# Kernel tuning notes

Hardware: AMD Instinct MI355X
Metric: run time of the kernel (lower is better)

## Reference

```python
import jax, jax.numpy as jnp
import numpy as np

N = 100000
E = 1250000
H = 64


def setup_inputs() -> dict:
    key = jax.random.key(0)
    ks = jax.random.split(key, 20)
    x = jax.random.normal(ks[0], (N, 1), dtype=jnp.float32)
    edge_index = jax.random.randint(ks[1], (2, E), 0, N, dtype=jnp.int64)
    edge_attr = jax.random.uniform(ks[2], (E,), dtype=jnp.float32)
    def lin(k, fin, fout):
        s = 1.0 / np.sqrt(fin)
        kw, kb = jax.random.split(k)
        W = jax.random.uniform(kw, (fin, fout), minval=-s, maxval=s, dtype=jnp.float32)
        b = jax.random.uniform(kb, (fout,), minval=-s, maxval=s, dtype=jnp.float32)
        return W, b
    W1, b1 = lin(ks[3], 1, H)
    W2, b2 = lin(ks[4], H, H)
    W3, b3 = lin(ks[5], H, H)
    W4, b4 = lin(ks[6], H, H)
    W5, b5 = lin(ks[7], H, H)
    fW1, fb1 = lin(ks[8], H, H)
    fW2, fb2 = lin(ks[9], H, 1)
    return dict(x=x, edge_index=edge_index, edge_attr=edge_attr,
                W1=W1, b1=b1, W2=W2, b2=b2, W3=W3, b3=b3, W4=W4, b4=b4,
                W5=W5, b5=b5, fW1=fW1, fb1=fb1, fW2=fW2, fb2=fb2)


def _gcn_layer(x, W, b, src, dst, ew):
    # PyG GCNConv: x' = D^{-1/2}(A+I)D^{-1/2} x W + b (self-loops pre-appended)
    h = x @ W                                   # [N, H]
    deg = jax.ops.segment_sum(ew, dst, num_segments=N)
    dinv = jnp.where(deg > 0, jax.lax.rsqrt(deg), 0.0)
    norm = dinv[src] * ew * dinv[dst]           # [E+N]
    msg = h[src] * norm[:, None]                # [E+N, H]
    return jax.ops.segment_sum(msg, dst, num_segments=N) + b


def reference(x, edge_index, edge_attr, W1, b1, W2, b2, W3, b3, W4, b4, W5, b5, fW1, fb1, fW2, fb2):
    loops = jnp.arange(N, dtype=edge_index.dtype)
    src = jnp.concatenate([edge_index[0], loops])
    dst = jnp.concatenate([edge_index[1], loops])
    ew = jnp.concatenate([edge_attr, jnp.ones((N,), edge_attr.dtype)])
    h = jax.nn.relu(_gcn_layer(x, W1, b1, src, dst, ew))
    h = jax.nn.relu(_gcn_layer(h, W2, b2, src, dst, ew))
    h = jax.nn.relu(_gcn_layer(h, W3, b3, src, dst, ew))
    h = jax.nn.relu(_gcn_layer(h, W4, b4, src, dst, ew))
    h = jax.nn.relu(_gcn_layer(h, W5, b5, src, dst, ew))
    h = jax.nn.relu(h @ fW1 + fb1)
    return h @ fW2 + fb2
```

## Files before the change

kernel.cpp:

```cpp
#include <hip/hip_runtime.h>
#include <hip/hip_bf16.h>

#define NN 100000
#define EE 1250000

#define RL(x, l) __builtin_amdgcn_readlane((x), (l))
#define RLF(x, l) __int_as_float(__builtin_amdgcn_readlane(__float_as_int(x), (l)))

typedef __attribute__((ext_vector_type(8))) short v8s;
typedef __attribute__((ext_vector_type(4))) float v4f;
typedef __attribute__((ext_vector_type(4))) unsigned int v4u;

__device__ __forceinline__ unsigned short bf16rtn(float x) {
    unsigned u = __float_as_uint(x);
    unsigned r = u + 0x7fffu + ((u >> 16) & 1u);
    return (unsigned short)(r >> 16);
}
__device__ __forceinline__ unsigned bf16rtn2(float lo, float hi) {
    return (unsigned)bf16rtn(lo) | ((unsigned)bf16rtn(hi) << 16);
}
__device__ __forceinline__ float bflo(unsigned u) { return __uint_as_float(u << 16); }
__device__ __forceinline__ float bfhi(unsigned u) { return __uint_as_float(u & 0xffff0000u); }
__device__ __forceinline__ float bfs(unsigned short s) { return __uint_as_float((unsigned)s << 16); }


__global__ __launch_bounds__(256) void k_count(const int* __restrict__ ei,
                                               const float* __restrict__ ew,
                                               unsigned long long* __restrict__ cnt,
                                               int* __restrict__ slot) {
    int e = blockIdx.x * 256 + threadIdx.x;
    if (e >= EE) return;
    int d = __builtin_nontemporal_load(&ei[EE + e]);
    float w = __builtin_nontemporal_load(&ew[e]);
    unsigned fx = (unsigned)(w * 16777216.0f + 0.5f);
    unsigned long long old =
        atomicAdd(&cnt[d], (1ULL << 32) | (unsigned long long)fx);
    __builtin_nontemporal_store((int)(old >> 32), &slot[e]);
}

__global__ __launch_bounds__(256) void k_bsum(const unsigned long long* __restrict__ cnt,
                                              int* __restrict__ bsum) {
    __shared__ int ls[256];
    int b = blockIdx.x, tid = threadIdx.x;
    int base = b * 1024 + tid * 4;
    int s = 0;
    #pragma unroll
    for (int j = 0; j < 4; ++j) { int g = base + j; if (g < NN) s += (int)(cnt[g] >> 32); }
    ls[tid] = s; __syncthreads();
    for (int off = 128; off > 0; off >>= 1) {
        if (tid < off) ls[tid] += ls[tid + off];
        __syncthreads();
    }
    if (tid == 0) bsum[b] = ls[0];
}

__global__ __launch_bounds__(256) void k_scan_out(const unsigned long long* __restrict__ cnt,
                                                  const int* __restrict__ bsum,
                                                  const float* __restrict__ x,
                                                  int* __restrict__ rowptr,
                                                  float* __restrict__ dinv,
                                                  float* __restrict__ xd) {
    __shared__ int ls[256];
    __shared__ int sbase;
    int b = blockIdx.x, tid = threadIdx.x;
    if (tid < 64) {
        int w0 = (tid < b) ? bsum[tid] : 0;
        int w1 = ((64 + tid) < b) ? bsum[64 + tid] : 0;
        int s = w0 + w1;
        #pragma unroll
        for (int m = 32; m >= 1; m >>= 1) s += __shfl_xor(s, m, 64);
        if (tid == 0) sbase = s;
    }
    int base = b * 1024 + tid * 4;
    int c[4]; float sw[4]; int s = 0;
    #pragma unroll
    for (int j = 0; j < 4; ++j) {
        int g = base + j;
        unsigned long long v = (g < NN) ? cnt[g] : 0ULL;
        c[j] = (int)(v >> 32);
        sw[j] = (float)(unsigned)(v & 0xffffffffu) * (1.0f / 16777216.0f);
        s += c[j];
    }
    ls[tid] = s; __syncthreads();
    for (int off = 1; off < 256; off <<= 1) {
        int v = (tid >= off) ? ls[tid - off] : 0;
        __syncthreads();
        ls[tid] += v;
        __syncthreads();
    }
    int excl = ls[tid] - s + sbase;
    #pragma unroll
    for (int j = 0; j < 4; ++j) {
        int g = base + j;
        if (g < NN) {
            rowptr[g + 1] = excl + c[j];
            excl += c[j];
            float di = rsqrtf(sw[j] + 1.0f);
            dinv[g] = di;
            xd[g] = di * x[g];
        }
    }
    if (b == 0 && tid == 0) rowptr[0] = 0;
}

__global__ __launch_bounds__(256) void k_fill(const int* __restrict__ ei,
                                              const float* __restrict__ ew,
                                              const int* __restrict__ slot,
                                              const int* __restrict__ rowptr,
                                              int2* __restrict__ epair) {
    int e = blockIdx.x * 256 + threadIdx.x;
    if (e >= EE) return;
    int s = __builtin_nontemporal_load(&ei[e]);
    int d = __builtin_nontemporal_load(&ei[EE + e]);
    float w = __builtin_nontemporal_load(&ew[e]);
    int sl = __builtin_nontemporal_load(&slot[e]);
    int p = rowptr[d] + sl;
    epair[p] = make_int2(s, __float_as_int(w));
}

__global__ __launch_bounds__(256) void k_wpk(const float* __restrict__ Wa,
                                             const float* __restrict__ Wb,
                                             const float* __restrict__ Wc,
                                             const float* __restrict__ Wd,
                                             unsigned* __restrict__ Wf) {
    const float* W = (blockIdx.x == 0) ? Wa : (blockIdx.x == 1) ? Wb
                   : (blockIdx.x == 2) ? Wc : Wd;
    unsigned* out = Wf + blockIdx.x * 4096;
    int t = threadIdx.x;
    #pragma unroll
    for (int i = 0; i < 2; ++i) {
        int s = t * 2 + i;
        int lane = s & 63;
        int nt = (s >> 6) & 3;
        int kt = s >> 8;
        int col = nt * 16 + (lane & 15);
        int k0 = kt * 32 + (lane >> 4) * 8;
        unsigned hi[4], lo[4];
        #pragma unroll
        for (int d = 0; d < 4; ++d) {
            float w0 = W[(k0 + 2 * d) * 64 + col];
            float w1 = W[(k0 + 2 * d + 1) * 64 + col];
            unsigned short h0 = bf16rtn(w0), h1 = bf16rtn(w1);
            float r0 = w0 - bfs(h0), r1 = w1 - bfs(h1);
            hi[d] = (unsigned)h0 | ((unsigned)h1 << 16);
            lo[d] = (unsigned)bf16rtn(r0) | ((unsigned)bf16rtn(r1) << 16);
        }
        int gh = (0 * 2 + kt) * 4 + nt;
        int gl = (1 * 2 + kt) * 4 + nt;
        *(v4u*)&out[(gh * 64 + lane) * 4] = (v4u){hi[0], hi[1], hi[2], hi[3]};
        *(v4u*)&out[(gl * 64 + lane) * 4] = (v4u){lo[0], lo[1], lo[2], lo[3]};
    }
}


__global__ __launch_bounds__(256) void k_l1(
    const float* __restrict__ xd, const float* __restrict__ dinv,
    const int* __restrict__ rowptr, const int2* __restrict__ ep,
    const float* __restrict__ W1, const float* __restrict__ b1,
    const float* __restrict__ W2, unsigned short* __restrict__ Gout)
{
    __shared__ float sW[4096];
    int tid = threadIdx.x;
    #pragma unroll
    for (int i = 0; i < 16; ++i) sW[tid + i * 256] = W2[tid + i * 256];
    __syncthreads();
    int lane = tid & 63, l16 = lane & 15, sub = lane >> 4;
    int g4 = blockIdx.x * 4 + (tid >> 6);
    int nodeS = g4 * 4 + sub;
    int beg = rowptr[nodeS], end = rowptr[nodeS + 1];
    float partial = 0.f;
    for (int idx = beg + l16; idx < end; idx += 16) {
        int2 p = ep[idx];
        partial = fmaf(__int_as_float(p.y), xd[p.x], partial);
    }
    #pragma unroll
    for (int m = 8; m >= 1; m >>= 1) partial += __shfl_xor(partial, m, 64);
    float z = dinv[nodeS] * (xd[nodeS] + partial);
    float z0 = RLF(z, 0), z1 = RLF(z, 16), z2 = RLF(z, 32), z3 = RLF(z, 48);
    float w1l = W1[lane], b1l = b1[lane];
    float v0 = fmaxf(fmaf(z0, w1l, b1l), 0.f);
    float v1 = fmaxf(fmaf(z1, w1l, b1l), 0.f);
    float v2 = fmaxf(fmaf(z2, w1l, b1l), 0.f);
    float v3 = fmaxf(fmaf(z3, w1l, b1l), 0.f);
    float a0 = 0.f, a1 = 0.f, a2 = 0.f, a3 = 0.f;
    #pragma unroll
    for (int k = 0; k < 64; ++k) {
        float wk = sW[k * 64 + lane];
        a0 = fmaf(RLF(v0, k), wk, a0);
        a1 = fmaf(RLF(v1, k), wk, a1);
        a2 = fmaf(RLF(v2, k), wk, a2);
        a3 = fmaf(RLF(v3, k), wk, a3);
    }
    int n0 = g4 * 4;
    Gout[(n0 + 0) * 64 + lane] = bf16rtn(dinv[n0 + 0] * a0);
    Gout[(n0 + 1) * 64 + lane] = bf16rtn(dinv[n0 + 1] * a1);
    Gout[(n0 + 2) * 64 + lane] = bf16rtn(dinv[n0 + 2] * a2);
    Gout[(n0 + 3) * 64 + lane] = bf16rtn(dinv[n0 + 3] * a3);
}

__global__ __launch_bounds__(256) void k_gmv(
    const unsigned* __restrict__ G16, const float* __restrict__ dinv,
    const int* __restrict__ rowptr, const int2* __restrict__ ep,
    const float* __restrict__ bias, const unsigned* __restrict__ Wf,
    unsigned short* __restrict__ Gout)
{
    __shared__ __align__(16) unsigned sB[4096];
    __shared__ __align__(16) unsigned sA[4][128];
    int tid = threadIdx.x;
    #pragma unroll
    for (int i = 0; i < 4; ++i)
        ((v4u*)sB)[tid + i * 256] = ((const v4u*)Wf)[tid + i * 256];
    int lane = tid & 63;
    int wid  = tid >> 6;
    int lc   = lane & 31;
    int half = lane >> 5;
    int n0 = (blockIdx.x * 4 + wid) * 4;
    float2 bb = ((const float2*)bias)[lc];
    for (int r = 0; r < 4; ++r) {
        int node = n0 + r;
        int beg = __builtin_amdgcn_readfirstlane(rowptr[node]);
        int end = __builtin_amdgcn_readfirstlane(rowptr[node + 1]);
        float ax = 0.f, ay = 0.f;
        if (half == 0) {
            unsigned u = G16[node * 32 + lc];
            ax = bflo(u); ay = bfhi(u);
        }
        int j = beg;
        for (; j + 16 <= end; j += 16) {
            unsigned u[8]; float nv[8];
            #pragma unroll
            for (int t = 0; t < 8; ++t) {
                int2 pa = ep[j + t];
                int2 pb = ep[j + 8 + t];
                int src = half ? pb.x : pa.x;
                nv[t] = __int_as_float(half ? pb.y : pa.y);
                u[t] = G16[src * 32 + lc];
            }
            #pragma unroll
            for (int t = 0; t < 8; ++t) {
                ax = fmaf(bflo(u[t]), nv[t], ax);
                ay = fmaf(bfhi(u[t]), nv[t], ay);
            }
        }
        if (j < end) {
            unsigned u[8]; float nv[8];
            #pragma unroll
            for (int t = 0; t < 8; ++t) {
                int ia = j + t, ib = j + 8 + t;
                int2 pa = ep[ia < end ? ia : j];
                int2 pb = ep[ib < end ? ib : j];
                int src = half ? pb.x : pa.x;
                float w = __int_as_float(half ? pb.y : pa.y);
                bool v = half ? (ib < end) : (ia < end);
                nv[t] = v ? w : 0.f;
                u[t] = G16[src * 32 + lc];
            }
            #pragma unroll
            for (int t = 0; t < 8; ++t) {
                ax = fmaf(bflo(u[t]), nv[t], ax);
                ay = fmaf(bfhi(u[t]), nv[t], ay);
            }
        }
        ax += __shfl_xor(ax, 32, 64);
        ay += __shfl_xor(ay, 32, 64);
        float din = dinv[node];
        float ve = fmaxf(fmaf(din, ax, bb.x), 0.f);
        float vo = fmaxf(fmaf(din, ay, bb.y), 0.f);
        if (half == 0) sA[wid][r * 32 + lc] = bf16rtn2(ve, vo);
    }
    __syncthreads();
    int rr  = lane & 3;
    int blk = lane >> 4;
    v8s a0 = *(const v8s*)&sA[wid][rr * 32 +  0 + blk * 4];
    v8s a1 = *(const v8s*)&sA[wid][rr * 32 + 16 + blk * 4];
    v4f acc[4];
    #pragma unroll
    for (int nt = 0; nt < 4; ++nt) {
        v8s bh0 = *(const v8s*)&sB[((0 * 4 + nt) * 64 + lane) * 4];
        v8s bh1 = *(const v8s*)&sB[((1 * 4 + nt) * 64 + lane) * 4];
        v8s bl0 = *(const v8s*)&sB[((2 * 4 + nt) * 64 + lane) * 4];
        v8s bl1 = *(const v8s*)&sB[((3 * 4 + nt) * 64 + lane) * 4];
        v4f c = {0.f, 0.f, 0.f, 0.f};
        c = __builtin_amdgcn_mfma_f32_16x16x32_bf16(a0, bl0, c, 0, 0, 0);
        c = __builtin_amdgcn_mfma_f32_16x16x32_bf16(a1, bl1, c, 0, 0, 0);
        c = __builtin_amdgcn_mfma_f32_16x16x32_bf16(a0, bh0, c, 0, 0, 0);
        c = __builtin_amdgcn_mfma_f32_16x16x32_bf16(a1, bh1, c, 0, 0, 0);
        acc[nt] = c;
    }
    if (lane < 16) {
        float4 dn = *(const float4*)&dinv[n0];
        #pragma unroll
        for (int r = 0; r < 4; ++r) {
            float d = (r == 0) ? dn.x : (r == 1) ? dn.y : (r == 2) ? dn.z : dn.w;
            #pragma unroll
            for (int nt = 0; nt < 4; ++nt)
                Gout[(n0 + r) * 64 + nt * 16 + lane] = bf16rtn(d * acc[nt][r]);
        }
    }
}

__global__ __launch_bounds__(256) void k_ghead(
    const unsigned* __restrict__ G16, const float* __restrict__ dinv,
    const int* __restrict__ rowptr, const int2* __restrict__ ep,
    const float* __restrict__ b5, const unsigned* __restrict__ Wf,
    const float* __restrict__ fb1, const float* __restrict__ fW2,
    const float* __restrict__ fb2, float* __restrict__ out)
{
    __shared__ __align__(16) unsigned sB[4096];
    __shared__ __align__(16) unsigned sA[4][128];
    int tid = threadIdx.x;
    #pragma unroll
    for (int i = 0; i < 4; ++i)
        ((v4u*)sB)[tid + i * 256] = ((const v4u*)Wf)[tid + i * 256];
    int lane = tid & 63;
    int wid  = tid >> 6;
    int lc   = lane & 31;
    int half = lane >> 5;
    int n0 = (blockIdx.x * 4 + wid) * 4;
    float2 bb = ((const float2*)b5)[lc];
    int l16 = lane & 15;
    float fb1v[4], fw2v[4];
    #pragma unroll
    for (int nt = 0; nt < 4; ++nt) {
        fb1v[nt] = fb1[nt * 16 + l16];
        fw2v[nt] = fW2[nt * 16 + l16];
    }
    float fb2s = fb2[0];
    for (int r = 0; r < 4; ++r) {
        int node = n0 + r;
        int beg = __builtin_amdgcn_readfirstlane(rowptr[node]);
        int end = __builtin_amdgcn_readfirstlane(rowptr[node + 1]);
        float ax = 0.f, ay = 0.f;
        if (half == 0) {
            unsigned u = G16[node * 32 + lc];
            ax = bflo(u); ay = bfhi(u);
        }
        int j = beg;
        for (; j + 16 <= end; j += 16) {
            unsigned u[8]; float nv[8];
            #pragma unroll
            for (int t = 0; t < 8; ++t) {
                int2 pa = ep[j + t];
                int2 pb = ep[j + 8 + t];
                int src = half ? pb.x : pa.x;
                nv[t] = __int_as_float(half ? pb.y : pa.y);
                u[t] = G16[src * 32 + lc];
            }
            #pragma unroll
            for (int t = 0; t < 8; ++t) {
                ax = fmaf(bflo(u[t]), nv[t], ax);
                ay = fmaf(bfhi(u[t]), nv[t], ay);
            }
        }
        if (j < end) {
            unsigned u[8]; float nv[8];
            #pragma unroll
            for (int t = 0; t < 8; ++t) {
                int ia = j + t, ib = j + 8 + t;
                int2 pa = ep[ia < end ? ia : j];
                int2 pb = ep[ib < end ? ib : j];
                int src = half ? pb.x : pa.x;
                float w = __int_as_float(half ? pb.y : pa.y);
                bool v = half ? (ib < end) : (ia < end);
                nv[t] = v ? w : 0.f;
                u[t] = G16[src * 32 + lc];
            }
            #pragma unroll
            for (int t = 0; t < 8; ++t) {
                ax = fmaf(bflo(u[t]), nv[t], ax);
                ay = fmaf(bfhi(u[t]), nv[t], ay);
            }
        }
        ax += __shfl_xor(ax, 32, 64);
        ay += __shfl_xor(ay, 32, 64);
        float din = dinv[node];
        float ve = fmaxf(fmaf(din, ax, bb.x), 0.f);
        float vo = fmaxf(fmaf(din, ay, bb.y), 0.f);
        if (half == 0) sA[wid][r * 32 + lc] = bf16rtn2(ve, vo);
    }
    __syncthreads();
    int rr  = lane & 3;
    int blk = lane >> 4;
    v8s a0 = *(const v8s*)&sA[wid][rr * 32 +  0 + blk * 4];
    v8s a1 = *(const v8s*)&sA[wid][rr * 32 + 16 + blk * 4];
    v4f acc[4];
    #pragma unroll
    for (int nt = 0; nt < 4; ++nt) {
        v8s bh0 = *(const v8s*)&sB[((0 * 4 + nt) * 64 + lane) * 4];
        v8s bh1 = *(const v8s*)&sB[((1 * 4 + nt) * 64 + lane) * 4];
        v8s bl0 = *(const v8s*)&sB[((2 * 4 + nt) * 64 + lane) * 4];
        v8s bl1 = *(const v8s*)&sB[((3 * 4 + nt) * 64 + lane) * 4];
        v4f c = {0.f, 0.f, 0.f, 0.f};
        c = __builtin_amdgcn_mfma_f32_16x16x32_bf16(a0, bl0, c, 0, 0, 0);
        c = __builtin_amdgcn_mfma_f32_16x16x32_bf16(a1, bl1, c, 0, 0, 0);
        c = __builtin_amdgcn_mfma_f32_16x16x32_bf16(a0, bh0, c, 0, 0, 0);
        c = __builtin_amdgcn_mfma_f32_16x16x32_bf16(a1, bh1, c, 0, 0, 0);
        acc[nt] = c;
    }
    float tr[4];
    #pragma unroll
    for (int r = 0; r < 4; ++r) {
        float t = 0.f;
        #pragma unroll
        for (int nt = 0; nt < 4; ++nt)
            t += fmaxf(acc[nt][r] + fb1v[nt], 0.f) * fw2v[nt];
        #pragma unroll
        for (int m = 8; m >= 1; m >>= 1) t += __shfl_xor(t, m, 64);
        tr[r] = t;
    }
    if (lane == 0) {
        float4 o = {tr[0] + fb2s, tr[1] + fb2s, tr[2] + fb2s, tr[3] + fb2s};
        *(float4*)&out[n0] = o;
    }
}


extern "C" void kernel_launch(void* const* d_in, const int* in_sizes, int n_in,
                              void* d_out, int out_size, void* d_ws, size_t ws_size,
                              hipStream_t stream) {
    const float* x   = (const float*)d_in[0];
    const int*   ei  = (const int*)d_in[1];
    const float* ew  = (const float*)d_in[2];
    const float* W1  = (const float*)d_in[3];
    const float* b1  = (const float*)d_in[4];
    const float* W2  = (const float*)d_in[5];
    const float* b2  = (const float*)d_in[6];
    const float* W3  = (const float*)d_in[7];
    const float* b3  = (const float*)d_in[8];
    const float* W4  = (const float*)d_in[9];
    const float* b4  = (const float*)d_in[10];
    const float* W5  = (const float*)d_in[11];
    const float* b5  = (const float*)d_in[12];
    const float* fW1 = (const float*)d_in[13];
    const float* fb1 = (const float*)d_in[14];
    const float* fW2 = (const float*)d_in[15];
    const float* fb2 = (const float*)d_in[16];
    float* out = (float*)d_out;

    char* ws = (char*)d_ws;
    size_t o = 0;
    auto alloc = [&](size_t elems) -> void* {
        void* p = (void*)(ws + o);
        o += ((elems * 4 + 255) / 256) * 256;
        return p;
    };
    float* dinv   = (float*)alloc(NN);
    float* xd     = (float*)alloc(NN);
    int*   rowptr = (int*)alloc(NN + 1);
    unsigned long long* cnt64 = (unsigned long long*)alloc(2 * (size_t)NN);
    int*   bsum   = (int*)alloc(128);
    int2*  epair  = (int2*)alloc(2 * (size_t)EE);
    unsigned* Ga16 = (unsigned*)alloc((size_t)NN * 32);
    unsigned* Gb16 = (unsigned*)alloc((size_t)NN * 32);
    int*   slot   = (int*)alloc(EE);
    unsigned* Wf  = (unsigned*)alloc(4 * 4096);

    int gE  = (EE + 255) / 256;
    int nb  = (NN + 1023) / 1024;
    int gW4 = NN / 16;

    k_wpk<<<4, 256, 0, stream>>>(W3, W4, W5, fW1, Wf);
    hipMemsetAsync(cnt64, 0, NN * sizeof(unsigned long long), stream);
    k_count<<<gE, 256, 0, stream>>>(ei, ew, cnt64, slot);
    k_bsum<<<nb, 256, 0, stream>>>(cnt64, bsum);
    k_scan_out<<<nb, 256, 0, stream>>>(cnt64, bsum, x, rowptr, dinv, xd);
    k_fill<<<gE, 256, 0, stream>>>(ei, ew, slot, rowptr, epair);

    k_l1<<<gW4, 256, 0, stream>>>(xd, dinv, rowptr, epair, W1, b1, W2,
                                  (unsigned short*)Ga16);
    k_gmv<<<gW4, 256, 0, stream>>>(Ga16, dinv, rowptr, epair, b2, Wf + 0,
                                   (unsigned short*)Gb16);
    k_gmv<<<gW4, 256, 0, stream>>>(Gb16, dinv, rowptr, epair, b3, Wf + 4096,
                                   (unsigned short*)Ga16);
    k_gmv<<<gW4, 256, 0, stream>>>(Ga16, dinv, rowptr, epair, b4, Wf + 8192,
                                   (unsigned short*)Gb16);
    k_ghead<<<gW4, 256, 0, stream>>>(Gb16, dinv, rowptr, epair, b5, Wf + 12288,
                                     fb1, fW2, fb2, out);
}
```

Before: 428.0 us.

## Gather four nodes concurrently per wave with 16 lanes each and 8-byte loads

The aggregation in the middle layers and the head kernel is restructured. Each wave now processes its four nodes in parallel, one 16-lane quarter per node, with each lane loading 4 bf16 features (uint2). Before, the wave walked the nodes one after another, split edges across two 32-lane halves, and combined them with a cross-half shuffle. The aim is more memory parallelism and no serial per-node loop, at the cost of divergent loop trip counts when neighbouring nodes have different degrees.

```diff
diff --git a/kernel.cpp b/kernel.cpp
--- a/kernel.cpp
+++ b/kernel.cpp
@@ -152,6 +152,50 @@
     }
 }
 
+__device__ __forceinline__ void gatherq(
+    const unsigned* __restrict__ G16, const int2* __restrict__ ep,
+    int node, int beg, int end, int l16,
+    float& a0, float& a1, float& a2, float& a3)
+{
+    uint2 su = *(const uint2*)&G16[node * 32 + l16 * 2];
+    a0 = bflo(su.x); a1 = bfhi(su.x);
+    a2 = bflo(su.y); a3 = bfhi(su.y);
+    int j = beg;
+    for (; j + 8 <= end; j += 8) {
+        uint2 u[8]; float nv[8];
+        #pragma unroll
+        for (int t = 0; t < 8; ++t) {
+            int2 p = ep[j + t];
+            nv[t] = __int_as_float(p.y);
+            u[t] = *(const uint2*)&G16[p.x * 32 + l16 * 2];
+        }
+        #pragma unroll
+        for (int t = 0; t < 8; ++t) {
+            a0 = fmaf(bflo(u[t].x), nv[t], a0);
+            a1 = fmaf(bfhi(u[t].x), nv[t], a1);
+            a2 = fmaf(bflo(u[t].y), nv[t], a2);
+            a3 = fmaf(bfhi(u[t].y), nv[t], a3);
+        }
+    }
+    if (j < end) {
+        uint2 u[8]; float nv[8];
+        #pragma unroll
+        for (int t = 0; t < 8; ++t) {
+            int idx = j + t;
+            int2 p = ep[idx < end ? idx : j];
+            nv[t] = (idx < end) ? __int_as_float(p.y) : 0.f;
+            u[t] = *(const uint2*)&G16[p.x * 32 + l16 * 2];
+        }
+        #pragma unroll
+        for (int t = 0; t < 8; ++t) {
+            a0 = fmaf(bflo(u[t].x), nv[t], a0);
+            a1 = fmaf(bfhi(u[t].x), nv[t], a1);
+            a2 = fmaf(bflo(u[t].y), nv[t], a2);
+            a3 = fmaf(bfhi(u[t].y), nv[t], a3);
+        }
+    }
+}
+
 
 __global__ __launch_bounds__(256) void k_l1(
     const float* __restrict__ xd, const float* __restrict__ dinv,
@@ -212,67 +256,26 @@
         ((v4u*)sB)[tid + i * 256] = ((const v4u*)Wf)[tid + i * 256];
     int lane = tid & 63;
     int wid  = tid >> 6;
-    int lc   = lane & 31;
-    int half = lane >> 5;
+    int q    = lane >> 4;
+    int l16  = lane & 15;
     int n0 = (blockIdx.x * 4 + wid) * 4;
-    float2 bb = ((const float2*)bias)[lc];
-    for (int r = 0; r < 4; ++r) {
-        int node = n0 + r;
-        int beg = __builtin_amdgcn_readfirstlane(rowptr[node]);
-        int end = __builtin_amdgcn_readfirstlane(rowptr[node + 1]);
-        float ax = 0.f, ay = 0.f;
-        if (half == 0) {
-            unsigned u = G16[node * 32 + lc];
-            ax = bflo(u); ay = bfhi(u);
-        }
-        int j = beg;
-        for (; j + 16 <= end; j += 16) {
-            unsigned u[8]; float nv[8];
-            #pragma unroll
-            for (int t = 0; t < 8; ++t) {
-                int2 pa = ep[j + t];
-                int2 pb = ep[j + 8 + t];
-                int src = half ? pb.x : pa.x;
-                nv[t] = __int_as_float(half ? pb.y : pa.y);
-                u[t] = G16[src * 32 + lc];
-            }
-            #pragma unroll
-            for (int t = 0; t < 8; ++t) {
-                ax = fmaf(bflo(u[t]), nv[t], ax);
-                ay = fmaf(bfhi(u[t]), nv[t], ay);
-            }
-        }
-        if (j < end) {
-            unsigned u[8]; float nv[8];
-            #pragma unroll
-            for (int t = 0; t < 8; ++t) {
-                int ia = j + t, ib = j + 8 + t;
-                int2 pa = ep[ia < end ? ia : j];
-                int2 pb = ep[ib < end ? ib : j];
-                int src = half ? pb.x : pa.x;
-                float w = __int_as_float(half ? pb.y : pa.y);
-                bool v = half ? (ib < end) : (ia < end);
-                nv[t] = v ? w : 0.f;
-                u[t] = G16[src * 32 + lc];
-            }
-            #pragma unroll
-            for (int t = 0; t < 8; ++t) {
-                ax = fmaf(bflo(u[t]), nv[t], ax);
-                ay = fmaf(bfhi(u[t]), nv[t], ay);
-            }
-        }
-        ax += __shfl_xor(ax, 32, 64);
-        ay += __shfl_xor(ay, 32, 64);
-        float din = dinv[node];
-        float ve = fmaxf(fmaf(din, ax, bb.x), 0.f);
-        float vo = fmaxf(fmaf(din, ay, bb.y), 0.f);
-        if (half == 0) sA[wid][r * 32 + lc] = bf16rtn2(ve, vo);
-    }
+    int node = n0 + q;
+    int beg = rowptr[node], end = rowptr[node + 1];
+    float a0, a1, a2, a3;
+    gatherq(G16, ep, node, beg, end, l16, a0, a1, a2, a3);
+    float din = dinv[node];
+    float4 bv = *(const float4*)&bias[l16 * 4];
+    float v0 = fmaxf(fmaf(din, a0, bv.x), 0.f);
+    float v1 = fmaxf(fmaf(din, a1, bv.y), 0.f);
+    float v2 = fmaxf(fmaf(din, a2, bv.z), 0.f);
+    float v3 = fmaxf(fmaf(din, a3, bv.w), 0.f);
+    *(uint2*)&sA[wid][q * 32 + l16 * 2] =
+        make_uint2(bf16rtn2(v0, v1), bf16rtn2(v2, v3));
     __syncthreads();
     int rr  = lane & 3;
     int blk = lane >> 4;
-    v8s a0 = *(const v8s*)&sA[wid][rr * 32 +  0 + blk * 4];
-    v8s a1 = *(const v8s*)&sA[wid][rr * 32 + 16 + blk * 4];
+    v8s fa0 = *(const v8s*)&sA[wid][rr * 32 +  0 + blk * 4];
+    v8s fa1 = *(const v8s*)&sA[wid][rr * 32 + 16 + blk * 4];
     v4f acc[4];
     #pragma unroll
     for (int nt = 0; nt < 4; ++nt) {
@@ -281,10 +284,10 @@
         v8s bl0 = *(const v8s*)&sB[((2 * 4 + nt) * 64 + lane) * 4];
         v8s bl1 = *(const v8s*)&sB[((3 * 4 + nt) * 64 + lane) * 4];
         v4f c = {0.f, 0.f, 0.f, 0.f};
-        c = __builtin_amdgcn_mfma_f32_16x16x32_bf16(a0, bl0, c, 0, 0, 0);
-        c = __builtin_amdgcn_mfma_f32_16x16x32_bf16(a1, bl1, c, 0, 0, 0);
-        c = __builtin_amdgcn_mfma_f32_16x16x32_bf16(a0, bh0, c, 0, 0, 0);
-        c = __builtin_amdgcn_mfma_f32_16x16x32_bf16(a1, bh1, c, 0, 0, 0);
+        c = __builtin_amdgcn_mfma_f32_16x16x32_bf16(fa0, bl0, c, 0, 0, 0);
+        c = __builtin_amdgcn_mfma_f32_16x16x32_bf16(fa1, bl1, c, 0, 0, 0);
+        c = __builtin_amdgcn_mfma_f32_16x16x32_bf16(fa0, bh0, c, 0, 0, 0);
+        c = __builtin_amdgcn_mfma_f32_16x16x32_bf16(fa1, bh1, c, 0, 0, 0);
         acc[nt] = c;
     }
     if (lane < 16) {
@@ -314,11 +317,10 @@
         ((v4u*)sB)[tid + i * 256] = ((const v4u*)Wf)[tid + i * 256];
     int lane = tid & 63;
     int wid  = tid >> 6;
-    int lc   = lane & 31;
-    int half = lane >> 5;
+    int q    = lane >> 4;
+    int l16  = lane & 15;
     int n0 = (blockIdx.x * 4 + wid) * 4;
-    float2 bb = ((const float2*)b5)[lc];
-    int l16 = lane & 15;
+    int node = n0 + q;
     float fb1v[4], fw2v[4];
     #pragma unroll
     for (int nt = 0; nt < 4; ++nt) {
@@ -326,63 +328,22 @@
         fw2v[nt] = fW2[nt * 16 + l16];
     }
     float fb2s = fb2[0];
-    for (int r = 0; r < 4; ++r) {
-        int node = n0 + r;
-        int beg = __builtin_amdgcn_readfirstlane(rowptr[node]);
-        int end = __builtin_amdgcn_readfirstlane(rowptr[node + 1]);
-        float ax = 0.f, ay = 0.f;
-        if (half == 0) {
-            unsigned u = G16[node * 32 + lc];
-            ax = bflo(u); ay = bfhi(u);
-        }
-        int j = beg;
-        for (; j + 16 <= end; j += 16) {
-            unsigned u[8]; float nv[8];
-            #pragma unroll
-            for (int t = 0; t < 8; ++t) {
-                int2 pa = ep[j + t];
-                int2 pb = ep[j + 8 + t];
-                int src = half ? pb.x : pa.x;
-                nv[t] = __int_as_float(half ? pb.y : pa.y);
-                u[t] = G16[src * 32 + lc];
-            }
-            #pragma unroll
-            for (int t = 0; t < 8; ++t) {
-                ax = fmaf(bflo(u[t]), nv[t], ax);
-                ay = fmaf(bfhi(u[t]), nv[t], ay);
-            }
-        }
-        if (j < end) {
-            unsigned u[8]; float nv[8];
-            #pragma unroll
-            for (int t = 0; t < 8; ++t) {
-                int ia = j + t, ib = j + 8 + t;
-                int2 pa = ep[ia < end ? ia : j];
-                int2 pb = ep[ib < end ? ib : j];
-                int src = half ? pb.x : pa.x;
-                float w = __int_as_float(half ? pb.y : pa.y);
-                bool v = half ? (ib < end) : (ia < end);
-                nv[t] = v ? w : 0.f;
-                u[t] = G16[src * 32 + lc];
-            }
-            #pragma unroll
-            for (int t = 0; t < 8; ++t) {
-                ax = fmaf(bflo(u[t]), nv[t], ax);
-                ay = fmaf(bfhi(u[t]), nv[t], ay);
-            }
-        }
-        ax += __shfl_xor(ax, 32, 64);
-        ay += __shfl_xor(ay, 32, 64);
-        float din = dinv[node];
-        float ve = fmaxf(fmaf(din, ax, bb.x), 0.f);
-        float vo = fmaxf(fmaf(din, ay, bb.y), 0.f);
-        if (half == 0) sA[wid][r * 32 + lc] = bf16rtn2(ve, vo);
-    }
+    int beg = rowptr[node], end = rowptr[node + 1];
+    float a0, a1, a2, a3;
+    gatherq(G16, ep, node, beg, end, l16, a0, a1, a2, a3);
+    float din = dinv[node];
+    float4 bv = *(const float4*)&b5[l16 * 4];
+    float v0 = fmaxf(fmaf(din, a0, bv.x), 0.f);
+    float v1 = fmaxf(fmaf(din, a1, bv.y), 0.f);
+    float v2 = fmaxf(fmaf(din, a2, bv.z), 0.f);
+    float v3 = fmaxf(fmaf(din, a3, bv.w), 0.f);
+    *(uint2*)&sA[wid][q * 32 + l16 * 2] =
+        make_uint2(bf16rtn2(v0, v1), bf16rtn2(v2, v3));
     __syncthreads();
     int rr  = lane & 3;
     int blk = lane >> 4;
-    v8s a0 = *(const v8s*)&sA[wid][rr * 32 +  0 + blk * 4];
-    v8s a1 = *(const v8s*)&sA[wid][rr * 32 + 16 + blk * 4];
+    v8s fa0 = *(const v8s*)&sA[wid][rr * 32 +  0 + blk * 4];
+    v8s fa1 = *(const v8s*)&sA[wid][rr * 32 + 16 + blk * 4];
     v4f acc[4];
     #pragma unroll
     for (int nt = 0; nt < 4; ++nt) {
@@ -391,10 +352,10 @@
         v8s bl0 = *(const v8s*)&sB[((2 * 4 + nt) * 64 + lane) * 4];
         v8s bl1 = *(const v8s*)&sB[((3 * 4 + nt) * 64 + lane) * 4];
         v4f c = {0.f, 0.f, 0.f, 0.f};
-        c = __builtin_amdgcn_mfma_f32_16x16x32_bf16(a0, bl0, c, 0, 0, 0);
-        c = __builtin_amdgcn_mfma_f32_16x16x32_bf16(a1, bl1, c, 0, 0, 0);
-        c = __builtin_amdgcn_mfma_f32_16x16x32_bf16(a0, bh0, c, 0, 0, 0);
-        c = __builtin_amdgcn_mfma_f32_16x16x32_bf16(a1, bh1, c, 0, 0, 0);
+        c = __builtin_amdgcn_mfma_f32_16x16x32_bf16(fa0, bl0, c, 0, 0, 0);
+        c = __builtin_amdgcn_mfma_f32_16x16x32_bf16(fa1, bl1, c, 0, 0, 0);
+        c = __builtin_amdgcn_mfma_f32_16x16x32_bf16(fa0, bh0, c, 0, 0, 0);
+        c = __builtin_amdgcn_mfma_f32_16x16x32_bf16(fa1, bh1, c, 0, 0, 0);
         acc[nt] = c;
     }
     float tr[4];
```

Result: faster. 399.7 us (-6.6%).
